# Kernel tuning notes

Hardware: AMD Instinct MI355X
Metric: run time of the kernel (lower is better)

## Reference

```python
import jax, jax.numpy as jnp
import numpy as np

EPS = 1e-5
WSZ = 8
DH = 32


def _ln_chan(x, g, b):
    # channel LayerNorm over dim=1 of (B,C,H,W), biased variance
    mu = jnp.mean(x, axis=1, keepdims=True)
    var = jnp.mean((x - mu) ** 2, axis=1, keepdims=True)
    return (x - mu) / jnp.sqrt(var + EPS) * g[None, :, None, None] + b[None, :, None, None]


def _conv_transpose2d(x, w, b, stride, pad):
    # torch ConvTranspose2d: w is (C_in, C_out, kh, kw)
    k = w.shape[2]
    wf = jnp.flip(w, (2, 3)).transpose(1, 0, 2, 3)  # (O, I, kh, kw)
    out = jax.lax.conv_general_dilated(
        x, wf, window_strides=(1, 1),
        padding=[(k - 1 - pad, k - 1 - pad)] * 2,
        lhs_dilation=(stride, stride),
        dimension_numbers=("NCHW", "OIHW", "NCHW"))
    return out + b[None, :, None, None]


def _rope_cs(wh, ww, dh, dtype):
    quarter = dh // 4
    freq = 1.0 / (10000.0 ** (jnp.arange(quarter, dtype=dtype) / quarter))
    th = jnp.arange(wh, dtype=dtype)[:, None] * freq          # (wh, q)
    tw = jnp.arange(ww, dtype=dtype)[:, None] * freq          # (ww, q)
    th = jnp.broadcast_to(th[:, None, :], (wh, ww, quarter)).reshape(wh * ww, quarter)
    tw = jnp.broadcast_to(tw[None, :, :], (wh, ww, quarter)).reshape(wh * ww, quarter)
    theta = jnp.concatenate([th, tw], axis=-1)                # (L, dh/2)
    cos = jnp.concatenate([jnp.cos(theta), jnp.cos(theta)], axis=-1)  # (L, dh)
    sin = jnp.concatenate([jnp.sin(theta), jnp.sin(theta)], axis=-1)
    return cos, sin


def _rot_half(x):
    x1, x2 = jnp.split(x, 2, axis=-1)
    return jnp.concatenate([-x2, x1], axis=-1)


def _attn_block(x, g, b, wqkv, wout, bout, shifted):
    B, C, H, W = x.shape
    heads = C // DH
    xn = _ln_chan(x, g, b)
    if shifted:
        xn = jnp.roll(xn, shift=(-(WSZ // 2), -(WSZ // 2)), axis=(2, 3))
    nh, nw = H // WSZ, W // WSZ
    # window partition: (B,C,H,W) -> (B*nh*nw, L, C), L = WSZ*WSZ
    t = xn.reshape(B, C, nh, WSZ, nw, WSZ).transpose(0, 2, 4, 3, 5, 1)
    t = t.reshape(B * nh * nw, WSZ * WSZ, C)
    qkv = t @ wqkv.T                                           # (Bw, L, 3C)
    q, k, v = jnp.split(qkv, 3, axis=-1)

    def split_heads(a):
        return a.reshape(a.shape[0], a.shape[1], heads, DH).transpose(0, 2, 1, 3)
    q, k, v = map(split_heads, (q, k, v))                      # (Bw, h, L, d)
    cos, sin = _rope_cs(WSZ, WSZ, DH, q.dtype)                 # (L, d)
    q = q * cos + _rot_half(q) * sin
    k = k * cos + _rot_half(k) * sin
    scale = DH ** -0.5
    att = jax.nn.softmax(jnp.einsum("bhid,bhjd->bhij", q * scale, k), axis=-1)
    out = jnp.einsum("bhij,bhjd->bhid", att, v)                # (Bw, h, L, d)
    out = out.transpose(0, 2, 1, 3).reshape(B * nh * nw, WSZ * WSZ, C)
    out = out @ wout.T + bout
    out = out.reshape(B, nh, nw, WSZ, WSZ, C).transpose(0, 5, 1, 3, 2, 4).reshape(B, C, H, W)
    if shifted:
        out = jnp.roll(out, shift=(WSZ // 2, WSZ // 2), axis=(2, 3))
    return out


def _ff(x, g, b, w1, b1, w2, b2):
    xn = _ln_chan(x, g, b)
    h = jnp.einsum("bchw,oc->bohw", xn, w1) + b1[None, :, None, None]
    h = jax.nn.gelu(h)
    return jnp.einsum("bchw,oc->bohw", h, w2) + b2[None, :, None, None]


def _forward(x, ct_w2, ct_b2, ct_w4, ct_b4,
             a1_g, a1_b, a1_wqkv, a1_wout, a1_bout,
             f1_g, f1_b, f1_w1, f1_b1, f1_w2, f1_b2,
             a2_g, a2_b, a2_wqkv, a2_wout, a2_bout,
             f2_g, f2_b, f2_w1, f2_b1, f2_w2, f2_b2):
    # CrossExpandLayer: kernels [2,4], stride 2, padding (k-2)//2
    y2 = _conv_transpose2d(x, ct_w2, ct_b2, stride=2, pad=0)
    y4 = _conv_transpose2d(x, ct_w4, ct_b4, stride=2, pad=1)
    h = jnp.concatenate([y2, y4], axis=1)                      # (B, dim_out, 2H, 2W)
    h = h + _attn_block(h, a1_g, a1_b, a1_wqkv, a1_wout, a1_bout, shifted=False)
    h = h + _ff(h, f1_g, f1_b, f1_w1, f1_b1, f1_w2, f1_b2)
    h = h + _attn_block(h, a2_g, a2_b, a2_wqkv, a2_wout, a2_bout, shifted=True)
    h = h + _ff(h, f2_g, f2_b, f2_w1, f2_b1, f2_w2, f2_b2)
    return h


def setup_inputs() -> dict:
    key = jax.random.key(0)
    ks = jax.random.split(key, 32)
    DIM_IN, DIM = 512, 256
    MULT = 4
    s = 0.02
    inp = {"x": jax.random.normal(ks[0], (2, DIM_IN, 64, 128), dtype=jnp.float32)}
    # CrossExpandLayer: dim_scales = [128, 128]
    inp["ct_w2"] = jax.random.normal(ks[1], (DIM_IN, DIM // 2, 2, 2), jnp.float32) * s
    inp["ct_b2"] = jnp.zeros((DIM // 2,), jnp.float32)
    inp["ct_w4"] = jax.random.normal(ks[2], (DIM_IN, DIM // 2, 4, 4), jnp.float32) * s
    inp["ct_b4"] = jnp.zeros((DIM // 2,), jnp.float32)
    for i, pre in enumerate(["a1", "a2"]):
        inp[pre + "_g"] = jnp.ones((DIM,), jnp.float32)
        inp[pre + "_b"] = jnp.zeros((DIM,), jnp.float32)
        inp[pre + "_wqkv"] = jax.random.normal(ks[3 + 2 * i], (3 * DIM, DIM), jnp.float32) * s
        inp[pre + "_wout"] = jax.random.normal(ks[4 + 2 * i], (DIM, DIM), jnp.float32) * s
        inp[pre + "_bout"] = jnp.zeros((DIM,), jnp.float32)
    for i, pre in enumerate(["f1", "f2"]):
        inp[pre + "_g"] = jnp.ones((DIM,), jnp.float32)
        inp[pre + "_b"] = jnp.zeros((DIM,), jnp.float32)
        inp[pre + "_w1"] = jax.random.normal(ks[10 + 2 * i], (MULT * DIM, DIM), jnp.float32) * s
        inp[pre + "_b1"] = jnp.zeros((MULT * DIM,), jnp.float32)
        inp[pre + "_w2"] = jax.random.normal(ks[11 + 2 * i], (DIM, MULT * DIM), jnp.float32) * s
        inp[pre + "_b2"] = jnp.zeros((DIM,), jnp.float32)
    return inp


def reference(x, ct_w2, ct_b2, ct_w4, ct_b4,
              a1_g, a1_b, a1_wqkv, a1_wout, a1_bout,
              f1_g, f1_b, f1_w1, f1_b1, f1_w2, f1_b2,
              a2_g, a2_b, a2_wqkv, a2_wout, a2_bout,
              f2_g, f2_b, f2_w1, f2_b1, f2_w2, f2_b2):
    return _forward(x, ct_w2, ct_b2, ct_w4, ct_b4,
                    a1_g, a1_b, a1_wqkv, a1_wout, a1_bout,
                    f1_g, f1_b, f1_w1, f1_b1, f1_w2, f1_b2,
                    a2_g, a2_b, a2_wqkv, a2_wout, a2_bout,
                    f2_g, f2_b, f2_w1, f2_b1, f2_w2, f2_b2)
```

## Files before the change

kernel.cpp:

```cpp
#include <hip/hip_runtime.h>
#include <hip/hip_bf16.h>
#include <math.h>

typedef __bf16 bf16_t;
typedef __bf16 bf16x8 __attribute__((ext_vector_type(8)));
typedef float  f32x4 __attribute__((ext_vector_type(4)));

constexpr int B_  = 2;
constexpr int CIN = 512, HI = 64, WI = 128;
constexpr int C_  = 256, H_ = 128, W_ = 256;
constexpr int NTOK = B_ * H_ * W_;
constexpr int NWIN = 1024;

__device__ __forceinline__ unsigned short f2bu(float x) {
    return __builtin_bit_cast(unsigned short, (bf16_t)x);
}

__global__ __launch_bounds__(256) void k_rope(float* __restrict__ rope) {
    int i = blockIdx.x * 256 + threadIdx.x;
    if (i >= 2048) return;
    int l = i >> 5, d = i & 31;
    int j = d & 15;
    int ly = l >> 3, lx = l & 7;
    float fr = powf(10000.f, -(float)(j & 7) / 8.f);
    float t = (j < 8 ? (float)ly : (float)lx) * fr;
    rope[i]        = cosf(t);
    rope[2048 + i] = sinf(t);
}

struct CvtSeg { const float* s; bf16_t* d; unsigned n; };
struct CvtParams { CvtSeg seg[8]; };

__global__ __launch_bounds__(256) void k_cvt(CvtParams P) {
    unsigned base = (blockIdx.x * 256u + threadIdx.x) * 4u;
    for (int s = 0; s < 8; s++) {
        unsigned n = P.seg[s].n;
        if (base < n) {
            float4 v = *(const float4*)(P.seg[s].s + base);
            ushort4 o;
            o.x = f2bu(v.x); o.y = f2bu(v.y); o.z = f2bu(v.z); o.w = f2bu(v.w);
            *(ushort4*)(P.seg[s].d + base) = o;
            return;
        }
        base -= n;
    }
}

__global__ __launch_bounds__(256) void k_trx(const float* __restrict__ x,
                                             bf16_t* __restrict__ xT) {
    __shared__ float t[64][65];
    int pos0 = blockIdx.x << 6;
    int ci0  = blockIdx.y << 6;
    int b    = blockIdx.z;
    int tid = threadIdx.x;
    int cpos = tid & 63, rb = tid >> 6;
    const float* src = x + ((size_t)(b * CIN + ci0) << 13) + pos0;
    #pragma unroll
    for (int i = 0; i < 16; i++) {
        int ci = rb + (i << 2);
        t[ci][cpos] = src[((size_t)ci << 13) + cpos];
    }
    __syncthreads();
    int row = tid >> 2, q = tid & 3;
    bf16_t* dst = xT + ((size_t)((b << 13) + pos0 + row) << 9) + ci0 + (q << 4);
    union { uint4 u[2]; unsigned short us[16]; } o;
    #pragma unroll
    for (int e = 0; e < 16; e++)
        o.us[e] = f2bu(t[(q << 4) + e][row]);
    *(uint4*)dst = o.u[0];
    *(uint4*)(dst + 8) = o.u[1];
}

__global__ __launch_bounds__(256) void k_bmat(const float* __restrict__ w2,
                                              const float* __restrict__ w4,
                                              const float* __restrict__ cb2,
                                              const float* __restrict__ cb4,
                                              bf16_t* __restrict__ B512,
                                              bf16_t* __restrict__ B2048,
                                              float* __restrict__ cbias) {
    int idx = blockIdx.x * 256 + threadIdx.x;
    if (idx < 262144) {
        int ci = idx & 511, o = (idx >> 9) & 127, p = idx >> 16;
        int rp = p >> 1, rq = p & 1;
        B512[idx] = (bf16_t)w2[((ci * 128 + o) * 2 + rp) * 2 + rq];
        if (idx < 256) cbias[idx] = idx < 128 ? cb2[idx] : cb4[idx - 128];
    } else {
        int i4 = idx - 262144;
        int k = i4 & 2047, o2 = (i4 >> 11) & 127, p = i4 >> 18;
        int ci = k & 511, t = k >> 9;
        int rp = p >> 1, rq = p & 1, a = t >> 1, c = t & 1;
        int kh = 3 - rp - 2 * a, kw = 3 - rq - 2 * c;
        B2048[i4] = (bf16_t)w4[((ci * 128 + o2) * 4 + kh) * 4 + kw];
    }
}

__device__ __forceinline__ int winmap_pos(int idx, int shift) {
    int win = idx >> 6, l = idx & 63;
    int b = win >> 9, wy = (win >> 5) & 15, wx = win & 31;
    int y = ((wy << 3) + (l >> 3) + shift) & 127;
    int x = ((wx << 3) + (l & 7) + shift) & 255;
    return (b << 15) + (y << 8) + x;
}

__device__ __forceinline__ float gelu_tanh(float x) {
    float u = 1.5957691216057308f * (x + 0.044715f * x * x * x);
    return x - x / (__expf(u) + 1.f);
}

__device__ __forceinline__ int swz(int row, int byteoff) {
    return (row << 7) + (byteoff ^ ((row & 7) << 4));
}

template<int MODE>
__device__ __forceinline__ void gemm_body(
    char* smem,
    const bf16_t* __restrict__ A, const bf16_t* __restrict__ Bw,
    const float* __restrict__ bias, bf16_t* __restrict__ Cb,
    float* __restrict__ Hres, const float* __restrict__ rope,
    int K, int ldc, int pshift, int colbase)
{
    char* Asb = smem;
    char* Bsb = smem + 16384;
    const int tid = threadIdx.x;

    int gx = gridDim.x;
    int bx = blockIdx.x, by = blockIdx.y;
    if ((gridDim.y & 7) == 0) {
        int lin = by * gx + bx;
        int grp = gx << 3;
        int q = lin / grp, r = lin - q * grp;
        by = (r & 7) + (q << 3);
        bx = r >> 3;
    }
    const int m0 = by << 7, n0 = bx << 7;

    const int w = tid >> 6, l = tid & 63;
    const int wm = (w >> 1) << 6, wn = (w & 1) << 6;
    const int r16 = l & 15, r4 = l >> 4;
    const int arow = tid >> 3, abyte = (tid & 7) << 4;

    const bf16_t* Ag = A + (size_t)(m0 + arow) * K + ((tid & 7) << 3);
    const bf16_t* Bg = Bw + (size_t)(n0 + arow) * K + ((tid & 7) << 3);

    f32x4 acc[4][4] = {};
    uint4 ra[4], rb[4];
    #pragma unroll
    for (int i = 0; i < 4; i++) {
        ra[i] = *(const uint4*)(Ag + (size_t)(i << 5) * K);
        rb[i] = *(const uint4*)(Bg + (size_t)(i << 5) * K);
    }
    for (int kt = 0; kt < K; kt += 64) {
        __syncthreads();
        #pragma unroll
        for (int i = 0; i < 4; i++) {
            *(uint4*)(Asb + swz(arow + (i << 5), abyte)) = ra[i];
            *(uint4*)(Bsb + swz(arow + (i << 5), abyte)) = rb[i];
        }
        __syncthreads();
        if (kt + 64 < K) {
            #pragma unroll
            for (int i = 0; i < 4; i++) {
                ra[i] = *(const uint4*)(Ag + (size_t)(i << 5) * K + kt + 64);
                rb[i] = *(const uint4*)(Bg + (size_t)(i << 5) * K + kt + 64);
            }
        }
        #pragma unroll
        for (int kk = 0; kk < 2; kk++) {
            bf16x8 af[4], bfr[4];
            #pragma unroll
            for (int f = 0; f < 4; f++)
                af[f] = *(const bf16x8*)(Asb + swz(wm + (f << 4) + r16, (kk << 6) + (r4 << 4)));
            #pragma unroll
            for (int f = 0; f < 4; f++)
                bfr[f] = *(const bf16x8*)(Bsb + swz(wn + (f << 4) + r16, (kk << 6) + (r4 << 4)));
            #pragma unroll
            for (int fm = 0; fm < 4; fm++)
                #pragma unroll
                for (int fn = 0; fn < 4; fn++)
                    acc[fm][fn] = __builtin_amdgcn_mfma_f32_16x16x32_bf16(
                        af[fm], bfr[fn], acc[fm][fn], 0, 0, 0);
        }
    }

    float* Lt = (float*)smem;
    const int wgrp = wn >> 6;
    #pragma unroll
    for (int p2 = 0; p2 < 2; p2++) {
        __syncthreads();
        if (wgrp == p2) {
            #pragma unroll
            for (int fm = 0; fm < 4; fm++) {
                int lrow = wm + (fm << 4) + (r4 << 2);
                #pragma unroll
                for (int fn = 0; fn < 4; fn++) {
                    f32x4 v = acc[fm][fn];
                    int lcol = (fn << 4) + r16;
                    #pragma unroll
                    for (int j = 0; j < 4; j++)
                        Lt[(lrow + j) * 72 + lcol] = v[j];
                }
            }
        }
        __syncthreads();
        if constexpr (MODE == 0) {
            const int c0 = (tid & 7) << 3;
            const int gcol = n0 + (p2 << 6) + c0;
            const int which = gcol >> 8;
            const int dbase = c0 & 31;
            const int pc = c0 ^ 16;
            const float sc = (which == 0) ? 0.17677669529663687f : 1.f;
            #pragma unroll
            for (int rnd = 0; rnd < 4; rnd++) {
                int row = (tid >> 3) + (rnd << 5);
                int lidx = (m0 + row) & 63;
                float vv[8];
                *(float4*)(vv)     = *(const float4*)(Lt + row * 72 + c0);
                *(float4*)(vv + 4) = *(const float4*)(Lt + row * 72 + c0 + 4);
                union { uint4 q; unsigned short us[8]; } o;
                if (which < 2) {
                    float pp[8];
                    *(float4*)(pp)     = *(const float4*)(Lt + row * 72 + pc);
                    *(float4*)(pp + 4) = *(const float4*)(Lt + row * 72 + pc + 4);
                    #pragma unroll
                    for (int i = 0; i < 8; i++) {
                        int d = dbase + i;
                        float cs = rope[lidx * 32 + d];
                        float sn = rope[2048 + lidx * 32 + d];
                        float rot = (d < 16) ? -pp[i] : pp[i];
                        o.us[i] = f2bu((vv[i] * cs + rot * sn) * sc);
                    }
                } else {
                    #pragma unroll
                    for (int i = 0; i < 8; i++) o.us[i] = f2bu(vv[i]);
                }
                *(uint4*)(Cb + (size_t)(m0 + row) * ldc + gcol) = o.q;
            }
        } else {
            const int c0 = (tid & 15) << 2;
            const int gcol = colbase + n0 + (p2 << 6) + c0;
            float bb[4];
            *(float4*)bb = *(const float4*)(bias + gcol);
            const int rp = pshift >> 1, rq = pshift & 1;
            #pragma unroll
            for (int rnd = 0; rnd < 8; rnd++) {
                int row = (tid >> 4) + (rnd << 4);
                float4 v = *(const float4*)(Lt + row * 72 + c0);
                int idx = m0 + row;
                int b = idx >> 13, u = (idx >> 7) & 63, vpos = idx & 127;
                int pos = (b << 15) + (((u << 1) + rp) << 8) + (vpos << 1) + rq;
                float* hp = Hres + ((size_t)pos << 8) + gcol;
                float4 r2;
                r2.x = v.x + bb[0]; r2.y = v.y + bb[1];
                r2.z = v.z + bb[2]; r2.w = v.w + bb[3];
                *(float4*)hp = r2;
            }
        }
    }
}

__global__ __launch_bounds__(256) void k_qkv_gemm(
    const bf16_t* __restrict__ A, const bf16_t* __restrict__ Bw,
    bf16_t* __restrict__ Cb, const float* __restrict__ rope, int K, int ldc) {
    __shared__ char smem[36864];
    gemm_body<0>(smem, A, Bw, nullptr, Cb, nullptr, rope, K, ldc, 0, 0);
}

__global__ __launch_bounds__(256) void k_conv2(
    const bf16_t* __restrict__ xT, const bf16_t* __restrict__ B512,
    const float* __restrict__ cbias, float* __restrict__ h_t) {
    __shared__ char smem[36864];
    int par = blockIdx.z;
    gemm_body<4>(smem, xT, B512 + ((size_t)par << 16), cbias, nullptr,
                 h_t, nullptr, 512, 0, par, 0);
}

__global__ __launch_bounds__(256) void k_conv4(const bf16_t* __restrict__ xT,
                                               const bf16_t* __restrict__ B2048,
                                               const float* __restrict__ cbias,
                                               float* __restrict__ h_t) {
    __shared__ char smem[36864];
    char* Asb = smem;
    char* Bsb = smem + 16384;
    const int tid = threadIdx.x;
    const int par = blockIdx.z;
    const int rp = par >> 1, rq = par & 1;
    const int m0 = blockIdx.y << 7;

    const int w = tid >> 6, l = tid & 63;
    const int wm = (w >> 1) << 6, wn = (w & 1) << 6;
    const int r16 = l & 15, r4 = l >> 4;
    const int arow = tid >> 3, abyte = (tid & 7) << 4;
    const int klane = (tid & 7) << 3;

    int mr_[4], u_[4], v_[4];
    #pragma unroll
    for (int i = 0; i < 4; i++) {
        mr_[i] = m0 + arow + (i << 5);
        u_[i] = (mr_[i] >> 7) & 63;
        v_[i] = mr_[i] & 127;
    }
    const bf16_t* Bp = B2048 + ((size_t)par << 18);

    auto loadA = [&](int c, uint4* r) {
        int t = c >> 3, ci0 = (c & 7) << 6;
        int dh = rp - 1 + (t >> 1), dw = rq - 1 + (t & 1);
        int off = (dh << 7) + dw;
        #pragma unroll
        for (int i = 0; i < 4; i++) {
            bool ok = ((unsigned)(u_[i] + dh) < (unsigned)HI) &&
                      ((unsigned)(v_[i] + dw) < (unsigned)WI);
            if (ok)
                r[i] = *(const uint4*)(xT + ((size_t)(mr_[i] + off) << 9) + ci0 + klane);
            else
                r[i] = uint4{0, 0, 0, 0};
        }
    };
    auto loadB = [&](int c, uint4* r) {
        #pragma unroll
        for (int i = 0; i < 4; i++)
            r[i] = *(const uint4*)(Bp + ((size_t)(arow + (i << 5)) << 11)
                                   + (c << 6) + klane);
    };

    f32x4 acc[4][4] = {};
    uint4 ra[4], rb[4];
    loadA(0, ra);
    loadB(0, rb);
    for (int c = 0; c < 32; c++) {
        __syncthreads();
        #pragma unroll
        for (int i = 0; i < 4; i++) {
            *(uint4*)(Asb + swz(arow + (i << 5), abyte)) = ra[i];
            *(uint4*)(Bsb + swz(arow + (i << 5), abyte)) = rb[i];
        }
        __syncthreads();
        if (c + 1 < 32) {
            loadA(c + 1, ra);
            loadB(c + 1, rb);
        }
        #pragma unroll
        for (int kk = 0; kk < 2; kk++) {
            bf16x8 af[4], bfr[4];
            #pragma unroll
            for (int f = 0; f < 4; f++)
                af[f] = *(const bf16x8*)(Asb + swz(wm + (f << 4) + r16, (kk << 6) + (r4 << 4)));
            #pragma unroll
            for (int f = 0; f < 4; f++)
                bfr[f] = *(const bf16x8*)(Bsb + swz(wn + (f << 4) + r16, (kk << 6) + (r4 << 4)));
            #pragma unroll
            for (int fm = 0; fm < 4; fm++)
                #pragma unroll
                for (int fn = 0; fn < 4; fn++)
                    acc[fm][fn] = __builtin_amdgcn_mfma_f32_16x16x32_bf16(
                        af[fm], bfr[fn], acc[fm][fn], 0, 0, 0);
        }
    }

    float* Lt = (float*)smem;
    const int wgrp = wn >> 6;
    #pragma unroll
    for (int p2 = 0; p2 < 2; p2++) {
        __syncthreads();
        if (wgrp == p2) {
            #pragma unroll
            for (int fm = 0; fm < 4; fm++) {
                int lrow = wm + (fm << 4) + (r4 << 2);
                #pragma unroll
                for (int fn = 0; fn < 4; fn++) {
                    f32x4 v = acc[fm][fn];
                    int lcol = (fn << 4) + r16;
                    #pragma unroll
                    for (int j = 0; j < 4; j++)
                        Lt[(lrow + j) * 72 + lcol] = v[j];
                }
            }
        }
        __syncthreads();
        const int c0 = (tid & 15) << 2;
        const int gcol = 128 + (p2 << 6) + c0;
        float bb[4];
        *(float4*)bb = *(const float4*)(cbias + gcol);
        #pragma unroll
        for (int rnd = 0; rnd < 8; rnd++) {
            int row = (tid >> 4) + (rnd << 4);
            float4 v = *(const float4*)(Lt + row * 72 + c0);
            int idx = m0 + row;
            int b = idx >> 13, u = (idx >> 7) & 63, vpos = idx & 127;
            int pos = (b << 15) + (((u << 1) + rp) << 8) + (vpos << 1) + rq;
            float* hp = h_t + ((size_t)pos << 8) + gcol;
            float4 r2;
            r2.x = v.x + bb[0]; r2.y = v.y + bb[1];
            r2.z = v.z + bb[2]; r2.w = v.w + bb[3];
            *(float4*)hp = r2;
        }
    }
}

__global__ __launch_bounds__(256) void k_attnp(const bf16_t* __restrict__ qkv,
                                               const bf16_t* __restrict__ wout,
                                               const float* __restrict__ bout,
                                               float* __restrict__ h_t,
                                               int win_base, int shift) {
    __shared__ char smem[18944];
    bf16_t* Vs = (bf16_t*)smem;
    const int tid = threadIdx.x;
    const int w = tid >> 6, l = tid & 63;
    const int r16 = l & 15, r4 = l >> 4;
    bf16_t* Ps = (bf16_t*)(smem + 4608) + w * 1152;
    bf16_t* Os = (bf16_t*)(smem + 13824) + w * 640;
    const int winl = blockIdx.x;
    const bf16_t* qb = qkv + ((size_t)winl << 6) * 768;

    f32x4 acc[16] = {};
    for (int h = 0; h < 8; h++) {
        const int ho = h << 5;
        __syncthreads();
        {
            int tok = tid >> 2, dq = (tid & 3) << 3;
            bf16x8 vv = *(const bf16x8*)(qb + tok * 768 + 512 + ho + dq);
            #pragma unroll
            for (int e = 0; e < 8; e++)
                Vs[(dq + e) * 68 + tok] = vv[e];
        }
        __syncthreads();
        bf16x8 qa = *(const bf16x8*)(qb + (w * 16 + r16) * 768 + ho + r4 * 8);
        f32x4 s[4];
        #pragma unroll
        for (int jt = 0; jt < 4; jt++) {
            f32x4 z = {};
            bf16x8 kb = *(const bf16x8*)(qb + (jt * 16 + r16) * 768 + 256 + ho + r4 * 8);
            s[jt] = __builtin_amdgcn_mfma_f32_16x16x32_bf16(qa, kb, z, 0, 0, 0);
        }
        #pragma unroll
        for (int j = 0; j < 4; j++) {
            float m = fmaxf(fmaxf(s[0][j], s[1][j]), fmaxf(s[2][j], s[3][j]));
            #pragma unroll
            for (int o = 8; o > 0; o >>= 1) m = fmaxf(m, __shfl_xor(m, o));
            float sum = 0.f;
            #pragma unroll
            for (int jt = 0; jt < 4; jt++) { s[jt][j] = __expf(s[jt][j] - m); sum += s[jt][j]; }
            #pragma unroll
            for (int o = 8; o > 0; o >>= 1) sum += __shfl_xor(sum, o);
            float inv = 1.f / sum;
            #pragma unroll
            for (int jt = 0; jt < 4; jt++)
                Ps[(r4 * 4 + j) * 72 + jt * 16 + r16] = (bf16_t)(s[jt][j] * inv);
        }
        f32x4 ov[2] = {};
        #pragma unroll
        for (int kt = 0; kt < 2; kt++) {
            bf16x8 pa = *(const bf16x8*)(Ps + r16 * 72 + kt * 32 + r4 * 8);
            #pragma unroll
            for (int nt = 0; nt < 2; nt++) {
                bf16x8 vb = *(const bf16x8*)(Vs + (nt * 16 + r16) * 68 + kt * 32 + r4 * 8);
                ov[nt] = __builtin_amdgcn_mfma_f32_16x16x32_bf16(pa, vb, ov[nt], 0, 0, 0);
            }
        }
        #pragma unroll
        for (int nt = 0; nt < 2; nt++)
            #pragma unroll
            for (int j = 0; j < 4; j++)
                Os[(r4 * 4 + j) * 40 + nt * 16 + r16] = (bf16_t)ov[nt][j];
        bf16x8 oa = *(const bf16x8*)(Os + r16 * 40 + r4 * 8);
        #pragma unroll
        for (int nt = 0; nt < 16; nt++) {
            bf16x8 wb = *(const bf16x8*)(wout + (nt * 16 + r16) * 256 + ho + r4 * 8);
            acc[nt] = __builtin_amdgcn_mfma_f32_16x16x32_bf16(oa, wb, acc[nt], 0, 0, 0);
        }
    }

    float* Lt = (float*)smem;
    const int gwin = win_base + winl;
    #pragma unroll
    for (int p = 0; p < 4; p++) {
        __syncthreads();
        #pragma unroll
        for (int t2 = 0; t2 < 4; t2++) {
            f32x4 v = acc[p * 4 + t2];
            #pragma unroll
            for (int j = 0; j < 4; j++)
                Lt[(w * 16 + r4 * 4 + j) * 68 + t2 * 16 + r16] = v[j];
        }
        __syncthreads();
        int row = tid >> 2, c0 = (tid & 3) << 4;
        int pos = winmap_pos((gwin << 6) + row, shift);
        float* hp = h_t + ((size_t)pos << 8) + (p << 6) + c0;
        const float* bp = bout + (p << 6) + c0;
        #pragma unroll
        for (int i = 0; i < 4; i++) {
            float4 v = *(const float4*)(Lt + row * 68 + c0 + (i << 2));
            float4 bb = *(const float4*)(bp + (i << 2));
            float4 r = *(const float4*)(hp + (i << 2));
            r.x += v.x + bb.x; r.y += v.y + bb.y;
            r.z += v.z + bb.z; r.w += v.w + bb.w;
            *(float4*)(hp + (i << 2)) = r;
        }
    }
}

__global__ __launch_bounds__(256) void k_ffn(const bf16_t* __restrict__ xn,
                                             const bf16_t* __restrict__ w1,
                                             const float* __restrict__ b1,
                                             const bf16_t* __restrict__ w2,
                                             const float* __restrict__ b2,
                                             float* __restrict__ h_t) {
    __shared__ char smem[49152];
    bf16_t* Xs = (bf16_t*)smem;
    bf16_t* Hs = (bf16_t*)(smem + 32768);
    const int tid = threadIdx.x;
    const int w = tid >> 6, l = tid & 63;
    const int r16 = l & 15, r4 = l >> 4;
    const int tok0 = blockIdx.x << 6;

    const bf16_t* xsrc = xn + ((size_t)tok0 << 8);
    #pragma unroll
    for (int i = 0; i < 8; i++) {
        int gi = i * 256 + tid;
        int row = gi >> 5;
        int col = (gi & 31) << 3;
        uint4 v = *(const uint4*)(xsrc + gi * 8);
        *(uint4*)(Xs + (row << 8) + (col ^ ((row & 7) << 3))) = v;
    }
    __syncthreads();

    f32x4 acc2[4][4] = {};
    #pragma unroll
    for (int hc = 0; hc < 8; hc++) {
        f32x4 acc1[4][2] = {};
        #pragma unroll
        for (int kk = 0; kk < 8; kk++) {
            bf16x8 af[4];
            #pragma unroll
            for (int fm = 0; fm < 4; fm++)
                af[fm] = *(const bf16x8*)(Xs + (((fm << 4) + r16) << 8)
                          + (((kk << 5) + (r4 << 3)) ^ ((r16 & 7) << 3)));
            bf16x8 bf1[2];
            #pragma unroll
            for (int fn = 0; fn < 2; fn++) {
                int nh = (hc << 7) + (w << 5) + (fn << 4) + r16;
                bf1[fn] = *(const bf16x8*)(w1 + ((size_t)nh << 8) + (kk << 5) + (r4 << 3));
            }
            #pragma unroll
            for (int fm = 0; fm < 4; fm++)
                #pragma unroll
                for (int fn = 0; fn < 2; fn++)
                    acc1[fm][fn] = __builtin_amdgcn_mfma_f32_16x16x32_bf16(
                        af[fm], bf1[fn], acc1[fm][fn], 0, 0, 0);
        }
        if (hc) __syncthreads();
        #pragma unroll
        for (int fn = 0; fn < 2; fn++) {
            int hcol = (w << 5) + (fn << 4) + r16;
            float bi = b1[(hc << 7) + hcol];
            #pragma unroll
            for (int fm = 0; fm < 4; fm++) {
                #pragma unroll
                for (int j = 0; j < 4; j++) {
                    int row = (fm << 4) + (r4 << 2) + j;
                    Hs[(row << 7) + (hcol ^ ((row & 7) << 3))] =
                        (bf16_t)gelu_tanh(acc1[fm][fn][j] + bi);
                }
            }
        }
        __syncthreads();
        #pragma unroll
        for (int kk = 0; kk < 4; kk++) {
            bf16x8 a2[4];
            #pragma unroll
            for (int fm = 0; fm < 4; fm++)
                a2[fm] = *(const bf16x8*)(Hs + (((fm << 4) + r16) << 7)
                          + (((kk << 5) + (r4 << 3)) ^ ((r16 & 7) << 3)));
            bf16x8 b2f[4];
            #pragma unroll
            for (int fn = 0; fn < 4; fn++) {
                int nc = (w << 6) + (fn << 4) + r16;
                b2f[fn] = *(const bf16x8*)(w2 + ((size_t)nc << 10) + (hc << 7)
                           + (kk << 5) + (r4 << 3));
            }
            #pragma unroll
            for (int fm = 0; fm < 4; fm++)
                #pragma unroll
                for (int fn = 0; fn < 4; fn++)
                    acc2[fm][fn] = __builtin_amdgcn_mfma_f32_16x16x32_bf16(
                        a2[fm], b2f[fn], acc2[fm][fn], 0, 0, 0);
        }
    }

    float* Lt = (float*)smem;
    #pragma unroll
    for (int p = 0; p < 4; p++) {
        __syncthreads();
        if (w == p) {
            #pragma unroll
            for (int fm = 0; fm < 4; fm++)
                #pragma unroll
                for (int fn = 0; fn < 4; fn++) {
                    f32x4 v = acc2[fm][fn];
                    int col = (fn << 4) + r16;
                    #pragma unroll
                    for (int j = 0; j < 4; j++)
                        Lt[((fm << 4) + (r4 << 2) + j) * 68 + col] = v[j];
                }
        }
        __syncthreads();
        int row = tid >> 2;
        int c0 = (tid & 3) << 4;
        float* hp = h_t + (((size_t)(tok0 + row)) << 8) + (p << 6) + c0;
        const float* bp = b2 + (p << 6) + c0;
        #pragma unroll
        for (int i = 0; i < 4; i++) {
            float4 v = *(const float4*)(Lt + row * 68 + c0 + (i << 2));
            float4 bb = *(const float4*)(bp + (i << 2));
            float4 r = *(const float4*)(hp + (i << 2));
            r.x += v.x + bb.x; r.y += v.y + bb.y;
            r.z += v.z + bb.z; r.w += v.w + bb.w;
            *(float4*)(hp + (i << 2)) = r;
        }
    }
}

__global__ __launch_bounds__(256) void k_ln(const float* __restrict__ h,
                                            const float* __restrict__ g,
                                            const float* __restrict__ bt,
                                            bf16_t* __restrict__ xn,
                                            int windowed, int shift) {
    int tok = (blockIdx.x << 2) + (threadIdx.x >> 6);
    int l = threadIdx.x & 63;
    float4 v = *(const float4*)(h + ((size_t)tok << 8) + (l << 2));
    float s  = v.x + v.y + v.z + v.w;
    float s2 = v.x * v.x + v.y * v.y + v.z * v.z + v.w * v.w;
    #pragma unroll
    for (int o = 32; o > 0; o >>= 1) { s += __shfl_xor(s, o); s2 += __shfl_xor(s2, o); }
    float mu = s * (1.f / 256.f);
    float rs = rsqrtf(s2 * (1.f / 256.f) - mu * mu + 1e-5f);
    int orow = tok;
    if (windowed) {
        int b = tok >> 15, img = tok & 32767;
        int y2 = ((img >> 8) - shift) & 127;
        int x2 = ((img & 255) - shift) & 255;
        orow = (((b << 9) + ((y2 >> 3) << 5) + (x2 >> 3)) << 6) + ((y2 & 7) << 3) + (x2 & 7);
    }
    int c = l << 2;
    float4 gv = *(const float4*)(g + c);
    float4 bv = *(const float4*)(bt + c);
    ushort4 o;
    o.x = f2bu((v.x - mu) * rs * gv.x + bv.x);
    o.y = f2bu((v.y - mu) * rs * gv.y + bv.y);
    o.z = f2bu((v.z - mu) * rs * gv.z + bv.z);
    o.w = f2bu((v.w - mu) * rs * gv.w + bv.w);
    *(ushort4*)(xn + ((size_t)orow << 8) + c) = o;
}

__global__ __launch_bounds__(256) void k_tr(const float* __restrict__ src,
                                            float* __restrict__ dst) {
    __shared__ float t[64][65];
    int tx = blockIdx.x & 3;
    int ty = blockIdx.x >> 2;
    int tid = threadIdx.x;
    int c = (tx << 6) + (tid & 63), r = tid >> 6;
    #pragma unroll
    for (int i = 0; i < 16; i++)
        t[r + i * 4][tid & 63] = src[(size_t)((ty << 6) + r + i * 4) * 256 + c];
    __syncthreads();
    int tok = (ty << 6) + (tid & 63);
    int c2 = tid >> 6;
    #pragma unroll
    for (int i = 0; i < 16; i++)
        dst[(size_t)((tx << 6) + c2 + i * 4) * 32768 + tok] = t[tid & 63][c2 + i * 4];
}

__global__ __launch_bounds__(256) void k_tr2(const float* __restrict__ ht,
                                             float* __restrict__ out) {
    __shared__ float t[128][65];
    int tk0 = blockIdx.x << 7;
    int c0  = blockIdx.y << 6;
    int tid = threadIdx.x;
    #pragma unroll
    for (int rep = 0; rep < 8; rep++) {
        int idx = rep * 256 + tid;
        int row = idx >> 4, c4 = (idx & 15) << 2;
        float4 v = *(const float4*)(ht + ((size_t)(tk0 + row) << 8) + c0 + c4);
        t[row][c4] = v.x; t[row][c4 + 1] = v.y; t[row][c4 + 2] = v.z; t[row][c4 + 3] = v.w;
    }
    __syncthreads();
    int b = tk0 >> 15, img0 = tk0 & 32767;
    #pragma unroll
    for (int rep = 0; rep < 8; rep++) {
        int idx = rep * 256 + tid;
        int jc = idx & 31, c = idx >> 5;
        float4 v;
        v.x = t[(jc << 2) + 0][c];
        v.y = t[(jc << 2) + 1][c];
        v.z = t[(jc << 2) + 2][c];
        v.w = t[(jc << 2) + 3][c];
        *(float4*)(out + (((size_t)(b << 8) + c0 + c) << 15) + img0 + (jc << 2)) = v;
    }
}

extern "C" void kernel_launch(void* const* d_in, const int* in_sizes, int n_in,
                              void* d_out, int out_size, void* d_ws, size_t ws_size,
                              hipStream_t stream) {
    const float* x     = (const float*)d_in[0];
    const float* ct_w2 = (const float*)d_in[1];
    const float* ct_b2 = (const float*)d_in[2];
    const float* ct_w4 = (const float*)d_in[3];
    const float* ct_b4 = (const float*)d_in[4];
    const float* ag[2]  = {(const float*)d_in[5],  (const float*)d_in[10]};
    const float* abt[2] = {(const float*)d_in[6],  (const float*)d_in[11]};
    const float* awq[2] = {(const float*)d_in[7],  (const float*)d_in[12]};
    const float* awo[2] = {(const float*)d_in[8],  (const float*)d_in[13]};
    const float* abo[2] = {(const float*)d_in[9],  (const float*)d_in[14]};
    const float* fg[2]  = {(const float*)d_in[15], (const float*)d_in[21]};
    const float* fbt[2] = {(const float*)d_in[16], (const float*)d_in[22]};
    const float* fw1[2] = {(const float*)d_in[17], (const float*)d_in[23]};
    const float* fb1[2] = {(const float*)d_in[18], (const float*)d_in[24]};
    const float* fw2[2] = {(const float*)d_in[19], (const float*)d_in[25]};
    const float* fb2[2] = {(const float*)d_in[20], (const float*)d_in[26]};

    char* w = (char*)d_ws;
    auto alloc = [&](size_t bytes) {
        char* p = w; w += (bytes + 255) & ~(size_t)255; return p;
    };
    float*  rope  = (float*)alloc(4096 * 4);
    bf16_t* wqkvb[2] = {(bf16_t*)alloc(196608 * 2), (bf16_t*)alloc(196608 * 2)};
    bf16_t* woutb[2] = {(bf16_t*)alloc(65536 * 2),  (bf16_t*)alloc(65536 * 2)};
    bf16_t* fw1b[2]  = {(bf16_t*)alloc(262144 * 2), (bf16_t*)alloc(262144 * 2)};
    bf16_t* fw2b[2]  = {(bf16_t*)alloc(262144 * 2), (bf16_t*)alloc(262144 * 2)};
    bf16_t* B512  = (bf16_t*)alloc((size_t)262144 * 2);
    bf16_t* B2048 = (bf16_t*)alloc((size_t)1048576 * 2);
    float*  cbias = (float*)alloc(256 * 4);
    bf16_t* xT    = (bf16_t*)alloc((size_t)16384 * 512 * 2);
    char*   XN    = alloc(33554432);
    bf16_t* xn = (bf16_t*)XN;

    size_t usedB = (size_t)(w - (char*)d_ws);
    size_t rem = ws_size > usedB ? ws_size - usedB : 0;
    const size_t HT_BYTES = (size_t)NTOK * C_ * 4;
    bool pathA = rem >= HT_BYTES + (size_t)16777216;
    float* h_t = pathA ? (float*)alloc(HT_BYTES) : (float*)d_out;

    usedB = (size_t)(w - (char*)d_ws);
    size_t Sb = ws_size > usedB ? ws_size - usedB : 0;
    if (Sb > (size_t)134217728) Sb = 134217728;
    char* S = w;

    auto p2f = [](size_t v) -> size_t { size_t r = 1; while ((r << 1) <= v) r <<= 1; return r; };
    int CW = (int)(Sb / 98304 >= 1024 ? 1024 : p2f(Sb / 98304));
    if (CW < 16) CW = 16;

    k_rope<<<8, 256, 0, stream>>>(rope);
    CvtParams P;
    P.seg[0] = { awq[0],  wqkvb[0],  196608 };
    P.seg[1] = { awq[1],  wqkvb[1],  196608 };
    P.seg[2] = { awo[0],  woutb[0],  65536 };
    P.seg[3] = { awo[1],  woutb[1],  65536 };
    P.seg[4] = { fw1[0],  fw1b[0],   262144 };
    P.seg[5] = { fw1[1],  fw1b[1],   262144 };
    P.seg[6] = { fw2[0],  fw2b[0],   262144 };
    P.seg[7] = { fw2[1],  fw2b[1],   262144 };
    unsigned total4 = (196608u * 2 + 65536u * 2 + 262144u * 4) / 4;
    k_cvt<<<(total4 + 255) / 256, 256, 0, stream>>>(P);
    k_bmat<<<5120, 256, 0, stream>>>(ct_w2, ct_w4, ct_b2, ct_b4, B512, B2048, cbias);
    k_trx<<<dim3(128, 8, 2), 256, 0, stream>>>(x, xT);

    k_conv2<<<dim3(1, 128, 4), 256, 0, stream>>>(xT, B512, cbias, h_t);
    k_conv4<<<dim3(1, 128, 4), 256, 0, stream>>>(xT, B2048, cbias, h_t);

    for (int blk = 0; blk < 2; blk++) {
        int shift = blk ? 4 : 0;
        k_ln<<<NTOK / 4, 256, 0, stream>>>(h_t, ag[blk], abt[blk], xn, 1, shift);
        for (int w0 = 0; w0 < NWIN; w0 += CW) {
            bf16_t* qkvc = (bf16_t*)S;
            k_qkv_gemm<<<dim3(6, CW / 2), 256, 0, stream>>>(
                xn + (size_t)w0 * 64 * 256, wqkvb[blk], qkvc, rope, 256, 768);
            k_attnp<<<CW, 256, 0, stream>>>(qkvc, woutb[blk], abo[blk], h_t, w0, shift);
        }
        k_ln<<<NTOK / 4, 256, 0, stream>>>(h_t, fg[blk], fbt[blk], xn, 0, 0);
        k_ffn<<<NTOK / 64, 256, 0, stream>>>(xn, fw1b[blk], fb1[blk],
                                             fw2b[blk], fb2[blk], h_t);
    }

    if (pathA) {
        k_tr2<<<dim3(512, 4), 256, 0, stream>>>(h_t, (float*)d_out);
    } else {
        for (int b = 0; b < 2; b++) {
            hipMemcpyAsync(XN, h_t + (size_t)b * 32768 * 256, 33554432,
                           hipMemcpyDeviceToDevice, stream);
            k_tr<<<2048, 256, 0, stream>>>((const float*)XN,
                                           (float*)d_out + (size_t)b * 256 * 32768);
        }
    }
}
```

Before: 1.033 ms.

## Split FFN kernel work across 8 waves and use fast reciprocal in GELU

The fused FFN kernel now runs 512 threads (8 waves) per block instead of 256. Each wave owns half as many hidden columns in the first GEMM and half as many output columns in the second, which shrinks per-wave accumulators and should raise occupancy and latency hiding. The epilogue is reorganised to write two 128-column halves through a wider LDS staging tile. GELU also swaps the division for a hardware reciprocal approximation, which cuts ALU cost slightly at some precision loss. Each wave now loads fewer weight fragments per A fragment, so the A reads from LDS are reused less per MFMA.

```diff
diff --git a/kernel.cpp b/kernel.cpp
--- a/kernel.cpp
+++ b/kernel.cpp
@@ -104,7 +104,7 @@
 
 __device__ __forceinline__ float gelu_tanh(float x) {
     float u = 1.5957691216057308f * (x + 0.044715f * x * x * x);
-    return x - x / (__expf(u) + 1.f);
+    return x - x * __builtin_amdgcn_rcpf(__expf(u) + 1.f);
 }
 
 __device__ __forceinline__ int swz(int row, int byteoff) {
@@ -498,12 +498,12 @@
     }
 }
 
-__global__ __launch_bounds__(256) void k_ffn(const bf16_t* __restrict__ xn,
-                                             const bf16_t* __restrict__ w1,
-                                             const float* __restrict__ b1,
-                                             const bf16_t* __restrict__ w2,
-                                             const float* __restrict__ b2,
-                                             float* __restrict__ h_t) {
+__global__ __launch_bounds__(512, 6) void k_ffn(const bf16_t* __restrict__ xn,
+                                                const bf16_t* __restrict__ w1,
+                                                const float* __restrict__ b1,
+                                                const bf16_t* __restrict__ w2,
+                                                const float* __restrict__ b2,
+                                                float* __restrict__ h_t) {
     __shared__ char smem[49152];
     bf16_t* Xs = (bf16_t*)smem;
     bf16_t* Hs = (bf16_t*)(smem + 32768);
@@ -514,8 +514,8 @@
 
     const bf16_t* xsrc = xn + ((size_t)tok0 << 8);
     #pragma unroll
-    for (int i = 0; i < 8; i++) {
-        int gi = i * 256 + tid;
+    for (int i = 0; i < 4; i++) {
+        int gi = i * 512 + tid;
         int row = gi >> 5;
         int col = (gi & 31) << 3;
         uint4 v = *(const uint4*)(xsrc + gi * 8);
@@ -523,10 +523,10 @@
     }
     __syncthreads();
 
-    f32x4 acc2[4][4] = {};
+    f32x4 acc2[4][2] = {};
     #pragma unroll
     for (int hc = 0; hc < 8; hc++) {
-        f32x4 acc1[4][2] = {};
+        f32x4 acc1[4] = {};
         #pragma unroll
         for (int kk = 0; kk < 8; kk++) {
             bf16x8 af[4];
@@ -534,23 +534,16 @@
             for (int fm = 0; fm < 4; fm++)
                 af[fm] = *(const bf16x8*)(Xs + (((fm << 4) + r16) << 8)
                           + (((kk << 5) + (r4 << 3)) ^ ((r16 & 7) << 3)));
-            bf16x8 bf1[2];
-            #pragma unroll
-            for (int fn = 0; fn < 2; fn++) {
-                int nh = (hc << 7) + (w << 5) + (fn << 4) + r16;
-                bf1[fn] = *(const bf16x8*)(w1 + ((size_t)nh << 8) + (kk << 5) + (r4 << 3));
-            }
+            int nh = (hc << 7) + (w << 4) + r16;
+            bf16x8 bf1 = *(const bf16x8*)(w1 + ((size_t)nh << 8) + (kk << 5) + (r4 << 3));
             #pragma unroll
             for (int fm = 0; fm < 4; fm++)
-                #pragma unroll
-                for (int fn = 0; fn < 2; fn++)
-                    acc1[fm][fn] = __builtin_amdgcn_mfma_f32_16x16x32_bf16(
-                        af[fm], bf1[fn], acc1[fm][fn], 0, 0, 0);
+                acc1[fm] = __builtin_amdgcn_mfma_f32_16x16x32_bf16(
+                    af[fm], bf1, acc1[fm], 0, 0, 0);
         }
         if (hc) __syncthreads();
-        #pragma unroll
-        for (int fn = 0; fn < 2; fn++) {
-            int hcol = (w << 5) + (fn << 4) + r16;
+        {
+            int hcol = (w << 4) + r16;
             float bi = b1[(hc << 7) + hcol];
             #pragma unroll
             for (int fm = 0; fm < 4; fm++) {
@@ -558,7 +551,7 @@
                 for (int j = 0; j < 4; j++) {
                     int row = (fm << 4) + (r4 << 2) + j;
                     Hs[(row << 7) + (hcol ^ ((row & 7) << 3))] =
-                        (bf16_t)gelu_tanh(acc1[fm][fn][j] + bi);
+                        (bf16_t)gelu_tanh(acc1[fm][j] + bi);
                 }
             }
         }
@@ -570,17 +563,17 @@
             for (int fm = 0; fm < 4; fm++)
                 a2[fm] = *(const bf16x8*)(Hs + (((fm << 4) + r16) << 7)
                           + (((kk << 5) + (r4 << 3)) ^ ((r16 & 7) << 3)));
-            bf16x8 b2f[4];
-            #pragma unroll
-            for (int fn = 0; fn < 4; fn++) {
-                int nc = (w << 6) + (fn << 4) + r16;
+            bf16x8 b2f[2];
+            #pragma unroll
+            for (int fn = 0; fn < 2; fn++) {
+                int nc = (w << 5) + (fn << 4) + r16;
                 b2f[fn] = *(const bf16x8*)(w2 + ((size_t)nc << 10) + (hc << 7)
                            + (kk << 5) + (r4 << 3));
             }
             #pragma unroll
             for (int fm = 0; fm < 4; fm++)
                 #pragma unroll
-                for (int fn = 0; fn < 4; fn++)
+                for (int fn = 0; fn < 2; fn++)
                     acc2[fm][fn] = __builtin_amdgcn_mfma_f32_16x16x32_bf16(
                         a2[fm], b2f[fn], acc2[fm][fn], 0, 0, 0);
         }
@@ -588,28 +581,28 @@
 
     float* Lt = (float*)smem;
     #pragma unroll
-    for (int p = 0; p < 4; p++) {
-        __syncthreads();
-        if (w == p) {
+    for (int p = 0; p < 2; p++) {
+        __syncthreads();
+        if ((w >> 2) == p) {
             #pragma unroll
             for (int fm = 0; fm < 4; fm++)
                 #pragma unroll
-                for (int fn = 0; fn < 4; fn++) {
+                for (int fn = 0; fn < 2; fn++) {
                     f32x4 v = acc2[fm][fn];
-                    int col = (fn << 4) + r16;
+                    int col = ((w & 3) << 5) + (fn << 4) + r16;
                     #pragma unroll
                     for (int j = 0; j < 4; j++)
-                        Lt[((fm << 4) + (r4 << 2) + j) * 68 + col] = v[j];
+                        Lt[((fm << 4) + (r4 << 2) + j) * 132 + col] = v[j];
                 }
         }
         __syncthreads();
-        int row = tid >> 2;
-        int c0 = (tid & 3) << 4;
-        float* hp = h_t + (((size_t)(tok0 + row)) << 8) + (p << 6) + c0;
-        const float* bp = b2 + (p << 6) + c0;
+        int row = tid >> 3;
+        int c0 = (tid & 7) << 4;
+        float* hp = h_t + (((size_t)(tok0 + row)) << 8) + (p << 7) + c0;
+        const float* bp = b2 + (p << 7) + c0;
         #pragma unroll
         for (int i = 0; i < 4; i++) {
-            float4 v = *(const float4*)(Lt + row * 68 + c0 + (i << 2));
+            float4 v = *(const float4*)(Lt + row * 132 + c0 + (i << 2));
             float4 bb = *(const float4*)(bp + (i << 2));
             float4 r = *(const float4*)(hp + (i << 2));
             r.x += v.x + bb.x; r.y += v.y + bb.y;
@@ -776,7 +769,7 @@
             k_attnp<<<CW, 256, 0, stream>>>(qkvc, woutb[blk], abo[blk], h_t, w0, shift);
         }
         k_ln<<<NTOK / 4, 256, 0, stream>>>(h_t, fg[blk], fbt[blk], xn, 0, 0);
-        k_ffn<<<NTOK / 64, 256, 0, stream>>>(xn, fw1b[blk], fb1[blk],
+        k_ffn<<<NTOK / 64, 512, 0, stream>>>(xn, fw1b[blk], fb1[blk],
                                              fw2b[blk], fb2[blk], h_t);
     }
 
```

Measured after the change: 1.084 ms. +4.9%, slower.
